# Kernel optimization log

Hardware: AMD Instinct MI355X
Metric: run time of the kernel (lower is better)

The kernel has to match this reference:

```python
import jax, jax.numpy as jnp
import numpy as np

H = 768
L = 9
M = 5            # max_span_length
CTX_RATIO = 0.5
NEG_INF = -1e30


def setup_inputs() -> dict:
    key = jax.random.key(0)
    ks = jax.random.split(key, 12)
    B, S = 4, 2048
    sc = 1.0 / np.sqrt(H)
    return {
        "sequence_output": jax.random.normal(ks[0], (B, S, H), dtype=jnp.float32),
        "Wc": jax.random.normal(ks[1], (H, L), dtype=jnp.float32) * sc,
        "bc": jnp.zeros((L,), dtype=jnp.float32),
        "wa": jax.random.normal(ks[2], (H,), dtype=jnp.float32) * sc,
        "ba": jnp.zeros((), dtype=jnp.float32),
        "W1": jax.random.normal(ks[3], (2 * H, H), dtype=jnp.float32) * (1.0 / np.sqrt(2 * H)),
        "b1": jnp.zeros((H,), dtype=jnp.float32),
        "gamma": jnp.ones((H,), dtype=jnp.float32),
        "beta": jnp.zeros((H,), dtype=jnp.float32),
        "W2": jax.random.normal(ks[4], (H, L), dtype=jnp.float32) * sc,
        "b2": jnp.zeros((L,), dtype=jnp.float32),
    }


def reference(sequence_output, Wc, bc, wa, ba, W1, b1, gamma, beta, W2, b2):
    x = sequence_output                        # [B,S,H]
    B, S, _ = x.shape
    base_logits = jnp.einsum('bsh,hl->bsl', x, Wc) + bc   # [B,S,L]

    # sliding-window indices: window [i-M, i+M] clipped to [0, S)
    offsets = jnp.arange(-M, M + 1)            # [W]
    idx = jnp.arange(S)[:, None] + offsets     # [S,W]
    valid = (idx >= 0) & (idx < S)             # [S,W]
    idx_c = jnp.clip(idx, 0, S - 1)            # [S,W]

    # attention scores over window (span_attention linear -> scalar per token)
    scores = jnp.einsum('bsh,h->bs', x, wa) + ba           # [B,S]
    win_scores = scores[:, idx_c]                          # [B,S,W]
    win_scores = jnp.where(valid[None], win_scores, NEG_INF)
    attn = jax.nn.softmax(win_scores, axis=-1)             # [B,S,W]

    win_tokens = x[:, idx_c]                               # [B,S,W,H] gather
    weighted_ctx = jnp.einsum('bsw,bswh->bsh', attn, win_tokens)

    token_with_ctx = jnp.concatenate([x, weighted_ctx], axis=-1)  # [B,S,2H]
    h = jnp.einsum('bsd,dh->bsh', token_with_ctx, W1) + b1
    # LayerNorm (eps = 1e-5, torch default)
    mu = jnp.mean(h, axis=-1, keepdims=True)
    var = jnp.mean((h - mu) ** 2, axis=-1, keepdims=True)
    h = (h - mu) * jax.lax.rsqrt(var + 1e-5) * gamma + beta
    h = jax.nn.gelu(h, approximate=False)                  # torch nn.GELU default (erf)
    ctx_logits = jnp.einsum('bsh,hl->bsl', h, W2) + b2

    return (1.0 - CTX_RATIO) * base_logits + CTX_RATIO * ctx_logits
```

## Files before the change

### kernel.cpp

```cpp
#include <hip/hip_runtime.h>
#include <hip/hip_bf16.h>
#include <math.h>

#define S_LEN 2048
#define BATCH 4
#define HDIM 768
#define LOUT 9
#define NROWS (BATCH*S_LEN)
#define K2H 1536
#define WIN 11
#define NEG_INF_F (-1e30f)

typedef __attribute__((ext_vector_type(4))) float f32x4;
typedef __attribute__((ext_vector_type(8))) short bf16x8;

static __device__ __forceinline__ void async_ld16(const void* g, void* l) {
  __builtin_amdgcn_global_load_lds((const __attribute__((address_space(1))) void*)g,
                                   (__attribute__((address_space(3))) void*)l, 16, 0, 0);
}

static __device__ __forceinline__ unsigned short f2bf(float f) {
  union { float f; unsigned int u; } v; v.f = f;
  unsigned int u = v.u;
  unsigned int r = (u + 0x7fffu + ((u >> 16) & 1u)) >> 16;
  return (unsigned short)r;
}

static __device__ __forceinline__ float bf2f(unsigned short h) {
  union { unsigned int u; float f; } v; v.u = ((unsigned int)h) << 16;
  return v.f;
}

__global__ __launch_bounds__(256) void k_prep_w1t(const float* __restrict__ W1,
                                                  unsigned short* __restrict__ W1t) {
  __shared__ float tile[32][33];
  int bk = blockIdx.x % 48;
  int bn = blockIdx.x / 48;
  int tc = threadIdx.x % 32;
  int tr = threadIdx.x / 32;
  #pragma unroll
  for (int i = 0; i < 32; i += 8) {
    tile[tr + i][tc] = W1[(bk*32 + tr + i) * HDIM + bn*32 + tc];
  }
  __syncthreads();
  #pragma unroll
  for (int i = 0; i < 32; i += 8) {
    W1t[(bn*32 + tr + i) * K2H + bk*32 + tc] = f2bf(tile[tc][tr + i]);
  }
}

__global__ __launch_bounds__(192) void k_prep(const float* __restrict__ x,
                                              const float* __restrict__ wa,
                                              const float* __restrict__ ba,
                                              const float* __restrict__ Wc,
                                              const float* __restrict__ bc,
                                              unsigned short* __restrict__ xc,
                                              float* __restrict__ scores,
                                              float* __restrict__ base) {
  __shared__ float red[3][LOUT + 1];
  int bid = blockIdx.x;
  int row = (bid & 7) * 1024 + (bid >> 3);
  int t = threadIdx.x;
  int lane = t & 63, wave = t >> 6;
  const float4 v = *(const float4*)(x + row * HDIM + t * 4);
  const float4 w = *(const float4*)(wa + t * 4);
  ushort4 o;
  o.x = f2bf(v.x); o.y = f2bf(v.y); o.z = f2bf(v.z); o.w = f2bf(v.w);
  *(ushort4*)(xc + row * K2H + t * 4) = o;

  float pv[LOUT + 1];
  pv[LOUT] = v.x * w.x + v.y * w.y + v.z * w.z + v.w * w.w;
  #pragma unroll
  for (int l = 0; l < LOUT; ++l) pv[l] = 0.f;
  const float xvv[4] = { v.x, v.y, v.z, v.w };
  #pragma unroll
  for (int j = 0; j < 4; ++j) {
    const float* wr = Wc + (t * 4 + j) * LOUT;
    #pragma unroll
    for (int l = 0; l < LOUT; ++l) pv[l] += xvv[j] * wr[l];
  }
  #pragma unroll
  for (int l = 0; l <= LOUT; ++l)
    #pragma unroll
    for (int m = 1; m < 64; m <<= 1) pv[l] += __shfl_xor(pv[l], m);
  if (lane == 0) {
    #pragma unroll
    for (int l = 0; l <= LOUT; ++l) red[wave][l] = pv[l];
  }
  __syncthreads();
  if (t < LOUT) {
    base[row * LOUT + t] = red[0][t] + red[1][t] + red[2][t] + bc[t];
  } else if (t == LOUT) {
    scores[row] = red[0][LOUT] + red[1][LOUT] + red[2][LOUT] + ba[0];
  }
}

__global__ __launch_bounds__(192) void k_ctx(const float* __restrict__ scores,
                                             unsigned short* __restrict__ xc) {
  __shared__ float swin[WIN];
  int bid = blockIdx.x;
  int row = (bid & 7) * 1024 + (bid >> 3);
  int b = row >> 11, s = row & 2047;
  int t = threadIdx.x;
  if (t < WIN) {
    int j = s - 5 + t;
    bool valid = (j >= 0) && (j < S_LEN);
    int jc = valid ? j : (j < 0 ? 0 : S_LEN - 1);
    swin[t] = valid ? scores[b * S_LEN + jc] : NEG_INF_F;
  }
  __syncthreads();
  float mx = swin[0];
  #pragma unroll
  for (int w = 1; w < WIN; ++w) mx = fmaxf(mx, swin[w]);
  float es[WIN], ssum = 0.f;
  #pragma unroll
  for (int w = 0; w < WIN; ++w) {
    float sv = swin[w];
    es[w] = (sv > -1e29f) ? __expf(sv - mx) : 0.f;
    ssum += es[w];
  }
  float inv = 1.f / ssum;
  float c0 = 0.f, c1 = 0.f, c2 = 0.f, c3 = 0.f;
  #pragma unroll
  for (int w = 0; w < WIN; ++w) {
    float aw = es[w] * inv;
    int j = s - 5 + w;
    int jc = (j < 0) ? 0 : ((j >= S_LEN) ? S_LEN - 1 : j);
    const ushort4 uv = *(const ushort4*)(xc + (((long)b * S_LEN + jc) * K2H) + t * 4);
    c0 += aw * bf2f(uv.x);
    c1 += aw * bf2f(uv.y);
    c2 += aw * bf2f(uv.z);
    c3 += aw * bf2f(uv.w);
  }
  ushort4 o;
  o.x = f2bf(c0); o.y = f2bf(c1); o.z = f2bf(c2); o.w = f2bf(c3);
  *(ushort4*)(xc + row * K2H + HDIM + t * 4) = o;
}

__global__ __launch_bounds__(256, 2) void k_gemm(const unsigned short* __restrict__ A,
                                                 const unsigned short* __restrict__ Bt,
                                                 const float* __restrict__ b1,
                                                 unsigned short* __restrict__ Hout) {
  __shared__ unsigned short As[3][128 * 64];
  __shared__ unsigned short Bs[3][64 * 64];
  int bid = blockIdx.x;
  int obid = (bid & 7) * 96 + (bid >> 3);
  int bm = obid / 12, bn = obid % 12;
  int t = threadIdx.x;
  int lane = t & 63, wave = t >> 6;

  int rowc = lane >> 3;
  int slot = lane & 7;
  const unsigned short* gAj[4];
  #pragma unroll
  for (int j = 0; j < 4; ++j) {
    int rloc = j * 32 + wave * 8 + rowc;
    int f = (rloc ^ (rloc >> 3)) & 7;
    gAj[j] = A + (bm * 128 + rloc) * K2H + ((slot ^ f) & 7) * 8;
  }
  const unsigned short* gBj[2];
  #pragma unroll
  for (int j = 0; j < 2; ++j) {
    int rloc = j * 32 + wave * 8 + rowc;
    int f = (rloc ^ (rloc >> 3)) & 7;
    gBj[j] = Bt + (bn * 64 + rloc) * K2H + ((slot ^ f) & 7) * 8;
  }

  f32x4 acc[2][4] = {};

#define STAGE(buf, kt) do {                                                    \
    _Pragma("unroll")                                                          \
    for (int j = 0; j < 4; ++j)                                                \
      async_ld16(gAj[j] + (kt), &As[buf][(j * 32 + wave * 8) * 64]);           \
    _Pragma("unroll")                                                          \
    for (int j = 0; j < 2; ++j)                                                \
      async_ld16(gBj[j] + (kt), &Bs[buf][(j * 32 + wave * 8) * 64]);           \
  } while (0)

#define COMPUTE(buf) do {                                                      \
    const unsigned short* aB = &As[buf][0];                                    \
    const unsigned short* bB = &Bs[buf][0];                                    \
    _Pragma("unroll")                                                          \
    for (int kk = 0; kk < 2; ++kk) {                                           \
      bf16x8 af[2], bfv[4];                                                    \
      _Pragma("unroll")                                                        \
      for (int m = 0; m < 2; ++m) {                                            \
        int rl = wave * 32 + m * 16 + (lane & 15);                             \
        int f = (rl ^ (rl >> 3)) & 7;                                          \
        int sl = (kk * 4 + (lane >> 4)) ^ f;                                   \
        af[m] = *(const bf16x8*)(aB + rl * 64 + sl * 8);                       \
      }                                                                        \
      _Pragma("unroll")                                                        \
      for (int n = 0; n < 4; ++n) {                                            \
        int rl = n * 16 + (lane & 15);                                         \
        int f = (rl ^ (rl >> 3)) & 7;                                          \
        int sl = (kk * 4 + (lane >> 4)) ^ f;                                   \
        bfv[n] = *(const bf16x8*)(bB + rl * 64 + sl * 8);                      \
      }                                                                        \
      _Pragma("unroll")                                                        \
      for (int m = 0; m < 2; ++m)                                              \
        _Pragma("unroll")                                                      \
        for (int n = 0; n < 4; ++n)                                            \
          acc[m][n] = __builtin_amdgcn_mfma_f32_16x16x32_bf16(af[m], bfv[n], acc[m][n], 0, 0, 0); \
    }                                                                          \
  } while (0)

#define WBAR(n) asm volatile("s_waitcnt vmcnt(" #n ")\n\ts_barrier" ::: "memory")

  STAGE(0, 0);
  STAGE(1, 64);

  int bufc = 0;
  for (int tt = 0; tt < 22; ++tt) {
    WBAR(6);
    int bufn = bufc + 2; if (bufn >= 3) bufn -= 3;
    STAGE(bufn, (tt + 2) * 64);
    COMPUTE(bufc);
    bufc = (bufc == 2) ? 0 : bufc + 1;
  }
  WBAR(6);  COMPUTE(bufc);
  bufc = (bufc == 2) ? 0 : bufc + 1;
  WBAR(0);  COMPUTE(bufc);

  int orow = bm * 128 + wave * 32 + (lane >> 4) * 4;
  int ocol = bn * 64 + (lane & 15);
  #pragma unroll
  for (int m = 0; m < 2; ++m)
    #pragma unroll
    for (int n = 0; n < 4; ++n) {
      int col = ocol + n * 16;
      float bv = b1[col];
      #pragma unroll
      for (int r = 0; r < 4; ++r) {
        Hout[(orow + m * 16 + r) * HDIM + col] = f2bf(acc[m][n][r] + bv);
      }
    }
#undef STAGE
#undef COMPUTE
#undef WBAR
}

__global__ __launch_bounds__(192) void k_ln(const unsigned short* __restrict__ Hin,
                                            const float* __restrict__ gamma,
                                            const float* __restrict__ beta,
                                            const float* __restrict__ W2,
                                            const float* __restrict__ b2,
                                            const float* __restrict__ base,
                                            float* __restrict__ out) {
  __shared__ float redS[3], redQ[3], redp[3][LOUT];
  int row = blockIdx.x;
  int t = threadIdx.x;
  int lane = t & 63, wave = t >> 6;
  const ushort4 hv = *(const ushort4*)(Hin + row * HDIM + t * 4);
  const float vv[4] = { bf2f(hv.x), bf2f(hv.y), bf2f(hv.z), bf2f(hv.w) };
  float s1 = vv[0] + vv[1] + vv[2] + vv[3];
  float s2 = vv[0]*vv[0] + vv[1]*vv[1] + vv[2]*vv[2] + vv[3]*vv[3];
  #pragma unroll
  for (int m = 1; m < 64; m <<= 1) { s1 += __shfl_xor(s1, m); s2 += __shfl_xor(s2, m); }
  if (lane == 0) { redS[wave] = s1; redQ[wave] = s2; }
  __syncthreads();
  s1 = redS[0] + redS[1] + redS[2];
  s2 = redQ[0] + redQ[1] + redQ[2];
  float mu = s1 * (1.f / HDIM);
  float var = s2 * (1.f / HDIM) - mu * mu;
  float rstd = rsqrtf(var + 1e-5f);
  const float4 g4 = *(const float4*)(gamma + t * 4);
  const float4 be4 = *(const float4*)(beta + t * 4);
  const float gv[4] = { g4.x, g4.y, g4.z, g4.w };
  const float bv[4] = { be4.x, be4.y, be4.z, be4.w };
  float p[LOUT] = {};
  #pragma unroll
  for (int j = 0; j < 4; ++j) {
    float g = (vv[j] - mu) * rstd * gv[j] + bv[j];
    float gg = 0.5f * g * (1.f + erff(g * 0.70710678118654752f));
    const float* wrow = W2 + (t * 4 + j) * LOUT;
    #pragma unroll
    for (int l = 0; l < LOUT; ++l) p[l] += gg * wrow[l];
  }
  #pragma unroll
  for (int l = 0; l < LOUT; ++l)
    #pragma unroll
    for (int m = 1; m < 64; m <<= 1) p[l] += __shfl_xor(p[l], m);
  if (lane == 0) {
    #pragma unroll
    for (int l = 0; l < LOUT; ++l) redp[wave][l] = p[l];
  }
  __syncthreads();
  if (t < LOUT) {
    float cl = redp[0][t] + redp[1][t] + redp[2][t] + b2[t];
    out[row * LOUT + t] = 0.5f * base[row * LOUT + t] + 0.5f * cl;
  }
}

extern "C" void kernel_launch(void* const* d_in, const int* in_sizes, int n_in,
                              void* d_out, int out_size, void* d_ws, size_t ws_size,
                              hipStream_t stream) {
  const float* x     = (const float*)d_in[0];
  const float* Wc    = (const float*)d_in[1];
  const float* bc    = (const float*)d_in[2];
  const float* wa    = (const float*)d_in[3];
  const float* ba    = (const float*)d_in[4];
  const float* W1    = (const float*)d_in[5];
  const float* b1    = (const float*)d_in[6];
  const float* gamma = (const float*)d_in[7];
  const float* beta  = (const float*)d_in[8];
  const float* W2    = (const float*)d_in[9];
  const float* b2    = (const float*)d_in[10];
  float* out = (float*)d_out;

  char* ws = (char*)d_ws;
  unsigned short* xc  = (unsigned short*)(ws);
  unsigned short* w1t = (unsigned short*)(ws + 25165824);
  float* scores       = (float*)(ws + 27525120);
  float* base         = (float*)(ws + 27557888);
  unsigned short* hbuf = (unsigned short*)(ws + 27852800);

  k_prep_w1t<<<dim3(1152), dim3(256), 0, stream>>>(W1, w1t);
  k_prep    <<<dim3(8192), dim3(192), 0, stream>>>(x, wa, ba, Wc, bc, xc, scores, base);
  k_ctx     <<<dim3(8192), dim3(192), 0, stream>>>(scores, xc);
  k_gemm    <<<dim3(768),  dim3(256), 0, stream>>>(xc, w1t, b1, hbuf);
  k_ln      <<<dim3(8192), dim3(192), 0, stream>>>(hbuf, gamma, beta, W2, b2, base, out);
}
```

Before: 187.8 us.

## Shrink GEMM tiles to 64x64x32 with a 2x2 wave layout and more blocks

The W1 GEMM block tile drops from 128x64 with a K step of 64 to 64x64 with a K step of 32. The four waves are now arranged 2x2, each owning a 32x32 output sub-tile, and the launch grows from 768 to 1536 blocks. Occupancy hints rise to 6 blocks per CU, the LDS swizzle is reworked for 32-wide rows, and the K loop gets more iterations with partial unrolling. The aim is better CU occupancy and latency hiding on a GEMM that is small relative to the GPU. In exchange each MFMA has less data reuse, the A and B tiles are fetched from global memory more often, and barriers are more frequent.

```diff
diff --git a/kernel.cpp b/kernel.cpp
--- a/kernel.cpp
+++ b/kernel.cpp
@@ -137,97 +137,83 @@
   *(ushort4*)(xc + row * K2H + HDIM + t * 4) = o;
 }
 
-__global__ __launch_bounds__(256, 2) void k_gemm(const unsigned short* __restrict__ A,
+__global__ __launch_bounds__(256, 6) void k_gemm(const unsigned short* __restrict__ A,
                                                  const unsigned short* __restrict__ Bt,
                                                  const float* __restrict__ b1,
                                                  unsigned short* __restrict__ Hout) {
-  __shared__ unsigned short As[3][128 * 64];
-  __shared__ unsigned short Bs[3][64 * 64];
+  __shared__ unsigned short As[3][64 * 32];
+  __shared__ unsigned short Bs[3][64 * 32];
   int bid = blockIdx.x;
-  int obid = (bid & 7) * 96 + (bid >> 3);
+  int obid = (bid & 7) * 192 + (bid >> 3);
   int bm = obid / 12, bn = obid % 12;
   int t = threadIdx.x;
   int lane = t & 63, wave = t >> 6;
-
-  int rowc = lane >> 3;
-  int slot = lane & 7;
-  const unsigned short* gAj[4];
-  #pragma unroll
-  for (int j = 0; j < 4; ++j) {
-    int rloc = j * 32 + wave * 8 + rowc;
-    int f = (rloc ^ (rloc >> 3)) & 7;
-    gAj[j] = A + (bm * 128 + rloc) * K2H + ((slot ^ f) & 7) * 8;
-  }
-  const unsigned short* gBj[2];
-  #pragma unroll
-  for (int j = 0; j < 2; ++j) {
-    int rloc = j * 32 + wave * 8 + rowc;
-    int f = (rloc ^ (rloc >> 3)) & 7;
-    gBj[j] = Bt + (bn * 64 + rloc) * K2H + ((slot ^ f) & 7) * 8;
-  }
-
-  f32x4 acc[2][4] = {};
+  int wm = wave >> 1, wn = wave & 1;
+
+  int rST = wave * 16 + (lane >> 2);
+  int fST = (rST ^ (rST >> 2)) & 3;
+  int sST = ((lane & 3) ^ fST) & 3;
+  const unsigned short* gA = A  + (bm * 64 + rST) * K2H + sST * 8;
+  const unsigned short* gB = Bt + (bn * 64 + rST) * K2H + sST * 8;
+
+  int aoff[2], boff[2];
+  #pragma unroll
+  for (int m = 0; m < 2; ++m) {
+    int rl = wm * 32 + m * 16 + (lane & 15);
+    int f = (rl ^ (rl >> 2)) & 3;
+    aoff[m] = rl * 32 + (((lane >> 4) ^ f) & 3) * 8;
+  }
+  #pragma unroll
+  for (int n = 0; n < 2; ++n) {
+    int rl = wn * 32 + n * 16 + (lane & 15);
+    int f = (rl ^ (rl >> 2)) & 3;
+    boff[n] = rl * 32 + (((lane >> 4) ^ f) & 3) * 8;
+  }
+
+  f32x4 acc[2][2] = {};
 
 #define STAGE(buf, kt) do {                                                    \
+    async_ld16(gA + (kt), &As[buf][wave * 512]);                               \
+    async_ld16(gB + (kt), &Bs[buf][wave * 512]);                               \
+  } while (0)
+
+#define COMPUTE(buf) do {                                                      \
+    bf16x8 af[2], bfv[2];                                                      \
+    af[0] = *(const bf16x8*)(&As[buf][aoff[0]]);                               \
+    af[1] = *(const bf16x8*)(&As[buf][aoff[1]]);                               \
+    bfv[0] = *(const bf16x8*)(&Bs[buf][boff[0]]);                              \
+    bfv[1] = *(const bf16x8*)(&Bs[buf][boff[1]]);                              \
     _Pragma("unroll")                                                          \
-    for (int j = 0; j < 4; ++j)                                                \
-      async_ld16(gAj[j] + (kt), &As[buf][(j * 32 + wave * 8) * 64]);           \
-    _Pragma("unroll")                                                          \
-    for (int j = 0; j < 2; ++j)                                                \
-      async_ld16(gBj[j] + (kt), &Bs[buf][(j * 32 + wave * 8) * 64]);           \
+    for (int m = 0; m < 2; ++m)                                                \
+      _Pragma("unroll")                                                        \
+      for (int n = 0; n < 2; ++n)                                              \
+        acc[m][n] = __builtin_amdgcn_mfma_f32_16x16x32_bf16(af[m], bfv[n], acc[m][n], 0, 0, 0); \
   } while (0)
 
-#define COMPUTE(buf) do {                                                      \
-    const unsigned short* aB = &As[buf][0];                                    \
-    const unsigned short* bB = &Bs[buf][0];                                    \
-    _Pragma("unroll")                                                          \
-    for (int kk = 0; kk < 2; ++kk) {                                           \
-      bf16x8 af[2], bfv[4];                                                    \
-      _Pragma("unroll")                                                        \
-      for (int m = 0; m < 2; ++m) {                                            \
-        int rl = wave * 32 + m * 16 + (lane & 15);                             \
-        int f = (rl ^ (rl >> 3)) & 7;                                          \
-        int sl = (kk * 4 + (lane >> 4)) ^ f;                                   \
-        af[m] = *(const bf16x8*)(aB + rl * 64 + sl * 8);                       \
-      }                                                                        \
-      _Pragma("unroll")                                                        \
-      for (int n = 0; n < 4; ++n) {                                            \
-        int rl = n * 16 + (lane & 15);                                         \
-        int f = (rl ^ (rl >> 3)) & 7;                                          \
-        int sl = (kk * 4 + (lane >> 4)) ^ f;                                   \
-        bfv[n] = *(const bf16x8*)(bB + rl * 64 + sl * 8);                      \
-      }                                                                        \
-      _Pragma("unroll")                                                        \
-      for (int m = 0; m < 2; ++m)                                              \
-        _Pragma("unroll")                                                      \
-        for (int n = 0; n < 4; ++n)                                            \
-          acc[m][n] = __builtin_amdgcn_mfma_f32_16x16x32_bf16(af[m], bfv[n], acc[m][n], 0, 0, 0); \
-    }                                                                          \
-  } while (0)
-
 #define WBAR(n) asm volatile("s_waitcnt vmcnt(" #n ")\n\ts_barrier" ::: "memory")
 
   STAGE(0, 0);
-  STAGE(1, 64);
+  STAGE(1, 32);
 
   int bufc = 0;
-  for (int tt = 0; tt < 22; ++tt) {
-    WBAR(6);
+  #pragma unroll 3
+  for (int tt = 0; tt < 46; ++tt) {
+    WBAR(2);
     int bufn = bufc + 2; if (bufn >= 3) bufn -= 3;
-    STAGE(bufn, (tt + 2) * 64);
+    STAGE(bufn, (tt + 2) * 32);
     COMPUTE(bufc);
     bufc = (bufc == 2) ? 0 : bufc + 1;
   }
-  WBAR(6);  COMPUTE(bufc);
+  WBAR(2);  COMPUTE(bufc);
   bufc = (bufc == 2) ? 0 : bufc + 1;
   WBAR(0);  COMPUTE(bufc);
 
-  int orow = bm * 128 + wave * 32 + (lane >> 4) * 4;
-  int ocol = bn * 64 + (lane & 15);
+  int orow = bm * 64 + wm * 32 + (lane >> 4) * 4;
+  int ocol = bn * 64 + wn * 32 + (lane & 15);
   #pragma unroll
   for (int m = 0; m < 2; ++m)
     #pragma unroll
-    for (int n = 0; n < 4; ++n) {
+    for (int n = 0; n < 2; ++n) {
       int col = ocol + n * 16;
       float bv = b1[col];
       #pragma unroll
@@ -318,6 +304,6 @@
   k_prep_w1t<<<dim3(1152), dim3(256), 0, stream>>>(W1, w1t);
   k_prep    <<<dim3(8192), dim3(192), 0, stream>>>(x, wa, ba, Wc, bc, xc, scores, base);
   k_ctx     <<<dim3(8192), dim3(192), 0, stream>>>(scores, xc);
-  k_gemm    <<<dim3(768),  dim3(256), 0, stream>>>(xc, w1t, b1, hbuf);
+  k_gemm    <<<dim3(1536), dim3(256), 0, stream>>>(xc, w1t, b1, hbuf);
   k_ln      <<<dim3(8192), dim3(192), 0, stream>>>(hbuf, gamma, beta, W2, b2, base, out);
 }
```

New measurement: 185.3 us. Within noise of the previous version (-1.3%).
